# Kernel optimization log

Measured on AMD Instinct MI355X. Metric: run time of the kernel, lower is better.

Reference implementation:

```python
import jax, jax.numpy as jnp
import numpy as np

IDIM, HDIM, ODIM, G = 80, 512, 128, 5
B, T = 512, 512  # B = scan (time) axis of torch GRU (batch_first=False), T = GRU batch axis
P = G * 2 * ODIM + G  # 1285


def setup_inputs() -> dict:
    key = jax.random.key(0)
    ks = jax.random.split(key, 8)
    s = 0.05  # keep recurrent dynamics stable
    return {
        "ys": jax.random.normal(ks[0], (B, T, IDIM), jnp.float32),
        "W_ih": jax.random.normal(ks[1], (3 * HDIM, IDIM), jnp.float32) * s,
        "W_hh": jax.random.normal(ks[2], (3 * HDIM, HDIM), jnp.float32) * s,
        "b_ih": jax.random.normal(ks[3], (3 * HDIM,), jnp.float32) * s,
        "b_hh": jax.random.normal(ks[4], (3 * HDIM,), jnp.float32) * s,
        "W_proj": jax.random.normal(ks[5], (P, HDIM), jnp.float32) * s,
        "b_proj": jax.random.normal(ks[6], (P,), jnp.float32) * s,
        "eps": jax.random.normal(ks[7], (G, B, ODIM), jnp.float32),  # pre-drawn std-normal noise per component
    }


def _gru(ys, W_ih, W_hh, b_ih, b_hh):
    # torch GRU, batch_first=False: scan over axis 0 of ys, batch = axis 1.
    xp = jnp.einsum('btf,gf->btg', ys, W_ih) + b_ih  # (B, T, 3H), precomputed input projections
    h0 = jnp.zeros((ys.shape[1], HDIM), ys.dtype)

    def step(h, x):
        gh = h @ W_hh.T + b_hh
        xr, xz, xn = jnp.split(x, 3, axis=-1)
        hr, hz, hn = jnp.split(gh, 3, axis=-1)
        r = jax.nn.sigmoid(xr + hr)
        z = jax.nn.sigmoid(xz + hz)
        n = jnp.tanh(xn + r * hn)
        h_new = (1.0 - z) * n + z * h
        return h_new, h_new

    _, out = jax.lax.scan(step, h0, xp)  # (B, T, H)
    return out


def reference(ys, W_ih, W_hh, b_ih, b_hh, W_proj, b_proj, eps):
    out = _gru(ys, W_ih, W_hh, b_ih, b_hh)          # (B, T, H)
    last = out[:, -1, :]                             # (B, H), mirrors out[:, -1, :] in torch code
    params = last @ W_proj.T + b_proj                # (B, P)

    samples = jnp.zeros((ys.shape[0], ODIM), params.dtype)
    for i in range(G):  # tiny fixed component loop (G=5)
        mu = params[:, i * ODIM:(i + 1) * ODIM]                       # (B, odim)
        var = params[:, 2 * i * ODIM:(2 * i + 1) * ODIM] + 1e-6       # scale_tril diagonal == std
        s = jax.lax.stop_gradient(mu + var * eps[i])                  # MVN(mu, diag(var)^T diag(var)).sample()
        w = params[:, 2 * G * ODIM + i]                               # params[:, i - G]
        samples = samples + w[:, None] * s
    return samples[:, None, :]  # (B, 1, odim)
```

## Files before the change

### kernel.cpp

```cpp
#include <hip/hip_runtime.h>
#include <hip/hip_bf16.h>

#define IDIM 80
#define HDIM 512
#define ODIM 128
#define G5   5
#define BB   512
#define TT   512
#define PDIM 1285
#define GDIM 1536
#define NB   48
#define RPB  32

__device__ __forceinline__ void ag_store(float* p, float v) {
  __hip_atomic_store(p, v, __ATOMIC_RELAXED, __HIP_MEMORY_SCOPE_AGENT);
}
__device__ __forceinline__ float ag_load(const float* p) {
  return __hip_atomic_load(p, __ATOMIC_RELAXED, __HIP_MEMORY_SCOPE_AGENT);
}

__device__ __forceinline__ void grid_barrier(unsigned* bar, unsigned target) {
  __syncthreads();
  if (threadIdx.x == 0) {
    __hip_atomic_fetch_add(bar, 1u, __ATOMIC_ACQ_REL, __HIP_MEMORY_SCOPE_AGENT);
    while (__hip_atomic_load(bar, __ATOMIC_ACQUIRE, __HIP_MEMORY_SCOPE_AGENT) < target) {
      __builtin_amdgcn_s_sleep(1);
    }
  }
  __syncthreads();
}

__global__ void __launch_bounds__(512) gru_kernel(
    const float* __restrict__ ys, const float* __restrict__ W_ih,
    const float* __restrict__ W_hh, const float* __restrict__ b_ih,
    const float* __restrict__ b_hh,
    unsigned long long* ghT, float* xp, float* last, unsigned* bar)
{
  const int tid  = threadIdx.x;
  const int nb   = blockIdx.x;
  const int lane = tid & 63;
  const int wave = tid >> 6;
  const int r4   = lane >> 4;
  const int c    = lane & 15;
  const int row  = nb * RPB + wave * 4 + r4;

  __shared__ float hs[16 * 36];
  __shared__ float wih[32 * 82];
  __shared__ float bihs[32];

  float4 wreg[8];
  {
    const float4* wrow = (const float4*)(W_hh + (size_t)row * HDIM + c * 32);
    #pragma unroll
    for (int i = 0; i < 8; ++i) wreg[i] = wrow[i];
  }
  const float bhh_r = b_hh[row];

  for (int jj = tid; jj < 16 * 36; jj += 512) hs[jj] = 0.f;

  for (int idx = tid; idx < 32 * IDIM; idx += 512) {
    int g = idx / IDIM, f = idx % IDIM;
    wih[g * 82 + f] = W_ih[(size_t)(nb * RPB + g) * IDIM + f];
  }
  if (tid < 32) bihs[tid] = b_ih[nb * RPB + tid];
  __syncthreads();
  {
    const int g = tid & 31, b0 = tid >> 5;
    for (int pass = 0; pass < 32; ++pass) {
      int b = pass * 16 + b0;
      const float* yrow = ys + ((size_t)b * TT + (TT - 1)) * IDIM;
      float acc = bihs[g];
      #pragma unroll
      for (int f = 0; f < IDIM; f += 2) {
        float2 wv = *(const float2*)(&wih[g * 82 + f]);
        float2 yv = *(const float2*)(&yrow[f]);
        acc += wv.x * yv.x + wv.y * yv.y;
      }
      ag_store(&xp[(size_t)b * GDIM + nb * RPB + g], acc);
    }
  }
  grid_barrier(bar, NB * 1u);

  const int j = tid;
  const int jphys = (j >> 5) * 36 + (j & 31);

  for (int b = 0; b < BB; ++b) {
    const float* xpb = xp + (size_t)b * GDIM;
    float xr = ag_load(&xpb[j]);
    float xz = ag_load(&xpb[512 + j]);
    float xn = ag_load(&xpb[1024 + j]);

    const float4* hp = (const float4*)(hs + c * 36);
    float a0 = 0.f, a1 = 0.f, a2 = 0.f, a3 = 0.f;
    #pragma unroll
    for (int i = 0; i < 8; ++i) {
      float4 h4 = hp[i];
      a0 += wreg[i].x * h4.x; a1 += wreg[i].y * h4.y;
      a2 += wreg[i].z * h4.z; a3 += wreg[i].w * h4.w;
    }
    float acc = (a0 + a1) + (a2 + a3);
    acc += __shfl_xor(acc, 1);
    acc += __shfl_xor(acc, 2);
    acc += __shfl_xor(acc, 4);
    acc += __shfl_xor(acc, 8);
    unsigned long long* ghb = ghT + (size_t)(b & 1) * GDIM;
    if (c == 0) {
      union { float f; unsigned u; } cv; cv.f = acc + bhh_r;
      unsigned long long pv = ((unsigned long long)(unsigned)b << 32) | cv.u;
      __hip_atomic_store(&ghb[row], pv, __ATOMIC_RELAXED, __HIP_MEMORY_SCOPE_AGENT);
    }

    __syncthreads();

    float hr, hz, hn;
    {
      const unsigned long long* p0 = &ghb[j];
      const unsigned long long* p1 = &ghb[512 + j];
      const unsigned long long* p2 = &ghb[1024 + j];
      unsigned long long v0 = 0, v1 = 0, v2 = 0;
      bool d0 = false, d1 = false, d2 = false;
      int guard = 0;
      do {
        if (!d0) { v0 = __hip_atomic_load(p0, __ATOMIC_RELAXED, __HIP_MEMORY_SCOPE_AGENT);
                   d0 = ((unsigned)(v0 >> 32) == (unsigned)b); }
        if (!d1) { v1 = __hip_atomic_load(p1, __ATOMIC_RELAXED, __HIP_MEMORY_SCOPE_AGENT);
                   d1 = ((unsigned)(v1 >> 32) == (unsigned)b); }
        if (!d2) { v2 = __hip_atomic_load(p2, __ATOMIC_RELAXED, __HIP_MEMORY_SCOPE_AGENT);
                   d2 = ((unsigned)(v2 >> 32) == (unsigned)b); }
      } while ((!d0 || !d1 || !d2) && ++guard < (1 << 20));
      union { unsigned u; float f; } c0, c1, c2;
      c0.u = (unsigned)v0; c1.u = (unsigned)v1; c2.u = (unsigned)v2;
      hr = c0.f; hz = c1.f; hn = c2.f;
    }

    float h_old = hs[jphys];
    float r = 1.f / (1.f + __expf(-(xr + hr)));
    float z = 1.f / (1.f + __expf(-(xz + hz)));
    float e2 = __expf(2.f * (xn + r * hn));
    float n = 1.f - 2.f / (e2 + 1.f);
    float hnew = (1.f - z) * n + z * h_old;
    hs[jphys] = hnew;
    if (nb == 0) last[(size_t)b * HDIM + j] = hnew;
    __syncthreads();
  }
}

__global__ void __launch_bounds__(256) proj_kernel(
    const float* __restrict__ last, const float* __restrict__ W_proj,
    const float* __restrict__ b_proj, float* __restrict__ params)
{
  const int tid = threadIdx.x;
  const int pt = blockIdx.x * 64;
  const int bt = blockIdx.y * 64;
  __shared__ float As[16 * 65];
  __shared__ float Bs[16 * 65];
  const int tb = (tid >> 4) * 4;
  const int tp = (tid & 15) * 4;
  float acc[4][4] = {};
  for (int k0 = 0; k0 < HDIM; k0 += 16) {
    #pragma unroll
    for (int i = 0; i < 4; ++i) {
      int idx = tid + i * 256;
      int k = idx & 15, m = idx >> 4;
      As[k * 65 + m] = last[(size_t)(bt + m) * HDIM + k0 + k];
      int gp = pt + m;
      Bs[k * 65 + m] = (gp < PDIM) ? W_proj[(size_t)gp * HDIM + k0 + k] : 0.f;
    }
    __syncthreads();
    #pragma unroll
    for (int k = 0; k < 16; ++k) {
      float a[4], bv[4];
      #pragma unroll
      for (int i = 0; i < 4; ++i) a[i] = As[k * 65 + tb + i];
      #pragma unroll
      for (int i = 0; i < 4; ++i) bv[i] = Bs[k * 65 + tp + i];
      #pragma unroll
      for (int i = 0; i < 4; ++i)
        #pragma unroll
        for (int jj = 0; jj < 4; ++jj) acc[i][jj] += a[i] * bv[jj];
    }
    __syncthreads();
  }
  #pragma unroll
  for (int i = 0; i < 4; ++i) {
    int gb = bt + tb + i;
    #pragma unroll
    for (int jj = 0; jj < 4; ++jj) {
      int gp = pt + tp + jj;
      if (gp < PDIM) params[(size_t)gb * PDIM + gp] = acc[i][jj] + b_proj[gp];
    }
  }
}

__global__ void mix_kernel(const float* __restrict__ params,
                           const float* __restrict__ eps,
                           float* __restrict__ out)
{
  int b = blockIdx.x, o = threadIdx.x;
  const float* pr = params + (size_t)b * PDIM;
  float s = 0.f;
  #pragma unroll
  for (int i = 0; i < G5; ++i) {
    float mu  = pr[i * ODIM + o];
    float var = pr[2 * i * ODIM + o] + 1e-6f;
    float w   = pr[2 * G5 * ODIM + i];
    float e   = eps[((size_t)i * BB + b) * ODIM + o];
    s += w * (mu + var * e);
  }
  out[(size_t)b * ODIM + o] = s;
}

extern "C" void kernel_launch(void* const* d_in, const int* in_sizes, int n_in,
                              void* d_out, int out_size, void* d_ws, size_t ws_size,
                              hipStream_t stream) {
  const float* ys     = (const float*)d_in[0];
  const float* W_ih   = (const float*)d_in[1];
  const float* W_hh   = (const float*)d_in[2];
  const float* b_ih   = (const float*)d_in[3];
  const float* b_hh   = (const float*)d_in[4];
  const float* W_proj = (const float*)d_in[5];
  const float* b_proj = (const float*)d_in[6];
  const float* eps    = (const float*)d_in[7];
  float* out = (float*)d_out;

  char* ws = (char*)d_ws;
  unsigned* bar           = (unsigned*)ws;
  unsigned long long* ghT = (unsigned long long*)(ws + 256);
  float* xp     = (float*)(ws + 256 + 2 * GDIM * 8);
  float* last   = xp + (size_t)BB * GDIM;
  float* params = last + (size_t)BB * HDIM;

  hipMemsetAsync(bar, 0, 256, stream);
  hipMemsetAsync(ghT, 0xFF, 2 * GDIM * 8, stream);

  gru_kernel<<<NB, 512, 0, stream>>>(ys, W_ih, W_hh, b_ih, b_hh,
                                     ghT, xp, last, bar);

  dim3 gc((PDIM + 63) / 64, BB / 64);
  proj_kernel<<<gc, 256, 0, stream>>>(last, W_proj, b_proj, params);

  mix_kernel<<<BB, ODIM, 0, stream>>>(params, eps, out);
}
```

Before: 1.119 ms.

## Fuse output projection into GRU recurrence using double-buffered hidden state

Drops the separate projection GEMM kernel and the 'last' buffer. Each GRU block now holds a slice of W_proj rows in registers and computes params for the previous timestep from the shared hidden state while it waits for the cross-block gate exchange. The hidden state is double-buffered in shared memory, which lets one __syncthreads per step be removed. The cost is more registers and extra per-step work inside the latency-bound recurrence loop, which may lengthen the critical path.

```diff
diff --git a/kernel.cpp b/kernel.cpp
--- a/kernel.cpp
+++ b/kernel.cpp
@@ -11,11 +11,18 @@
 #define GDIM 1536
 #define NB   48
 #define RPB  32
-
-__device__ __forceinline__ void ag_store(float* p, float v) {
+#define PCPB 27
+
+__device__ __forceinline__ void ag_storef(float* p, float v) {
   __hip_atomic_store(p, v, __ATOMIC_RELAXED, __HIP_MEMORY_SCOPE_AGENT);
 }
-__device__ __forceinline__ float ag_load(const float* p) {
+__device__ __forceinline__ float ag_loadf(const float* p) {
+  return __hip_atomic_load(p, __ATOMIC_RELAXED, __HIP_MEMORY_SCOPE_AGENT);
+}
+__device__ __forceinline__ void ag_storeu(unsigned long long* p, unsigned long long v) {
+  __hip_atomic_store(p, v, __ATOMIC_RELAXED, __HIP_MEMORY_SCOPE_AGENT);
+}
+__device__ __forceinline__ unsigned long long ag_loadu(const unsigned long long* p) {
   return __hip_atomic_load(p, __ATOMIC_RELAXED, __HIP_MEMORY_SCOPE_AGENT);
 }
 
@@ -33,8 +40,10 @@
 __global__ void __launch_bounds__(512) gru_kernel(
     const float* __restrict__ ys, const float* __restrict__ W_ih,
     const float* __restrict__ W_hh, const float* __restrict__ b_ih,
-    const float* __restrict__ b_hh,
-    unsigned long long* ghT, float* xp, float* last, unsigned* bar)
+    const float* __restrict__ b_hh, const float* __restrict__ W_proj,
+    const float* __restrict__ b_proj,
+    float* __restrict__ xp, unsigned long long* __restrict__ ghT,
+    float* __restrict__ params, unsigned* __restrict__ bar)
 {
   const int tid  = threadIdx.x;
   const int nb   = blockIdx.x;
@@ -44,7 +53,7 @@
   const int c    = lane & 15;
   const int row  = nb * RPB + wave * 4 + r4;
 
-  __shared__ float hs[16 * 36];
+  __shared__ float hs[2][16 * 36];
   __shared__ float wih[32 * 82];
   __shared__ float bihs[32];
 
@@ -56,7 +65,19 @@
   }
   const float bhh_r = b_hh[row];
 
-  for (int jj = tid; jj < 16 * 36; jj += 512) hs[jj] = 0.f;
+  const int pcol = nb * PCPB + (tid >> 4);
+  const int pcl  = tid & 15;
+  const bool pact = (tid < 16 * PCPB) && (pcol < PDIM);
+  float4 wp[8] = {};
+  float bp = 0.f;
+  if (pact) {
+    const float4* wrow = (const float4*)(W_proj + (size_t)pcol * HDIM + pcl * 32);
+    #pragma unroll
+    for (int i = 0; i < 8; ++i) wp[i] = wrow[i];
+    bp = b_proj[pcol];
+  }
+
+  for (int w = tid; w < 16 * 36; w += 512) { hs[0][w] = 0.f; hs[1][w] = 0.f; }
 
   for (int idx = tid; idx < 32 * IDIM; idx += 512) {
     int g = idx / IDIM, f = idx % IDIM;
@@ -76,7 +97,7 @@
         float2 yv = *(const float2*)(&yrow[f]);
         acc += wv.x * yv.x + wv.y * yv.y;
       }
-      ag_store(&xp[(size_t)b * GDIM + nb * RPB + g], acc);
+      ag_storef(&xp[(size_t)b * GDIM + nb * RPB + g], acc);
     }
   }
   grid_barrier(bar, NB * 1u);
@@ -86,15 +107,15 @@
 
   for (int b = 0; b < BB; ++b) {
     const float* xpb = xp + (size_t)b * GDIM;
-    float xr = ag_load(&xpb[j]);
-    float xz = ag_load(&xpb[512 + j]);
-    float xn = ag_load(&xpb[1024 + j]);
-
-    const float4* hp = (const float4*)(hs + c * 36);
+    float xr = ag_loadf(&xpb[j]);
+    float xz = ag_loadf(&xpb[512 + j]);
+    float xn = ag_loadf(&xpb[1024 + j]);
+
+    const float* hbase = &hs[b & 1][c * 36];
     float a0 = 0.f, a1 = 0.f, a2 = 0.f, a3 = 0.f;
     #pragma unroll
     for (int i = 0; i < 8; ++i) {
-      float4 h4 = hp[i];
+      float4 h4 = ((const float4*)hbase)[i];
       a0 += wreg[i].x * h4.x; a1 += wreg[i].y * h4.y;
       a2 += wreg[i].z * h4.z; a3 += wreg[i].w * h4.w;
     }
@@ -107,10 +128,25 @@
     if (c == 0) {
       union { float f; unsigned u; } cv; cv.f = acc + bhh_r;
       unsigned long long pv = ((unsigned long long)(unsigned)b << 32) | cv.u;
-      __hip_atomic_store(&ghb[row], pv, __ATOMIC_RELAXED, __HIP_MEMORY_SCOPE_AGENT);
-    }
-
-    __syncthreads();
+      ag_storeu(&ghb[row], pv);
+    }
+
+    if (b >= 1 && pact) {
+      const float* pb = &hs[b & 1][pcl * 36];
+      float p0 = 0.f, p1 = 0.f, p2 = 0.f, p3 = 0.f;
+      #pragma unroll
+      for (int i = 0; i < 8; ++i) {
+        float4 h4 = ((const float4*)pb)[i];
+        p0 += wp[i].x * h4.x; p1 += wp[i].y * h4.y;
+        p2 += wp[i].z * h4.z; p3 += wp[i].w * h4.w;
+      }
+      float pr = (p0 + p1) + (p2 + p3);
+      pr += __shfl_xor(pr, 1);
+      pr += __shfl_xor(pr, 2);
+      pr += __shfl_xor(pr, 4);
+      pr += __shfl_xor(pr, 8);
+      if (pcl == 0) params[(size_t)(b - 1) * PDIM + pcol] = pr + bp;
+    }
 
     float hr, hz, hn;
     {
@@ -121,74 +157,40 @@
       bool d0 = false, d1 = false, d2 = false;
       int guard = 0;
       do {
-        if (!d0) { v0 = __hip_atomic_load(p0, __ATOMIC_RELAXED, __HIP_MEMORY_SCOPE_AGENT);
-                   d0 = ((unsigned)(v0 >> 32) == (unsigned)b); }
-        if (!d1) { v1 = __hip_atomic_load(p1, __ATOMIC_RELAXED, __HIP_MEMORY_SCOPE_AGENT);
-                   d1 = ((unsigned)(v1 >> 32) == (unsigned)b); }
-        if (!d2) { v2 = __hip_atomic_load(p2, __ATOMIC_RELAXED, __HIP_MEMORY_SCOPE_AGENT);
-                   d2 = ((unsigned)(v2 >> 32) == (unsigned)b); }
+        if (!d0) { v0 = ag_loadu(p0); d0 = ((unsigned)(v0 >> 32) == (unsigned)b); }
+        if (!d1) { v1 = ag_loadu(p1); d1 = ((unsigned)(v1 >> 32) == (unsigned)b); }
+        if (!d2) { v2 = ag_loadu(p2); d2 = ((unsigned)(v2 >> 32) == (unsigned)b); }
       } while ((!d0 || !d1 || !d2) && ++guard < (1 << 20));
       union { unsigned u; float f; } c0, c1, c2;
       c0.u = (unsigned)v0; c1.u = (unsigned)v1; c2.u = (unsigned)v2;
       hr = c0.f; hz = c1.f; hn = c2.f;
     }
 
-    float h_old = hs[jphys];
+    float h_old = hs[b & 1][jphys];
     float r = 1.f / (1.f + __expf(-(xr + hr)));
     float z = 1.f / (1.f + __expf(-(xz + hz)));
     float e2 = __expf(2.f * (xn + r * hn));
     float n = 1.f - 2.f / (e2 + 1.f);
     float hnew = (1.f - z) * n + z * h_old;
-    hs[jphys] = hnew;
-    if (nb == 0) last[(size_t)b * HDIM + j] = hnew;
+    hs[(b + 1) & 1][jphys] = hnew;
     __syncthreads();
   }
-}
-
-__global__ void __launch_bounds__(256) proj_kernel(
-    const float* __restrict__ last, const float* __restrict__ W_proj,
-    const float* __restrict__ b_proj, float* __restrict__ params)
-{
-  const int tid = threadIdx.x;
-  const int pt = blockIdx.x * 64;
-  const int bt = blockIdx.y * 64;
-  __shared__ float As[16 * 65];
-  __shared__ float Bs[16 * 65];
-  const int tb = (tid >> 4) * 4;
-  const int tp = (tid & 15) * 4;
-  float acc[4][4] = {};
-  for (int k0 = 0; k0 < HDIM; k0 += 16) {
-    #pragma unroll
-    for (int i = 0; i < 4; ++i) {
-      int idx = tid + i * 256;
-      int k = idx & 15, m = idx >> 4;
-      As[k * 65 + m] = last[(size_t)(bt + m) * HDIM + k0 + k];
-      int gp = pt + m;
-      Bs[k * 65 + m] = (gp < PDIM) ? W_proj[(size_t)gp * HDIM + k0 + k] : 0.f;
-    }
-    __syncthreads();
-    #pragma unroll
-    for (int k = 0; k < 16; ++k) {
-      float a[4], bv[4];
-      #pragma unroll
-      for (int i = 0; i < 4; ++i) a[i] = As[k * 65 + tb + i];
-      #pragma unroll
-      for (int i = 0; i < 4; ++i) bv[i] = Bs[k * 65 + tp + i];
-      #pragma unroll
-      for (int i = 0; i < 4; ++i)
-        #pragma unroll
-        for (int jj = 0; jj < 4; ++jj) acc[i][jj] += a[i] * bv[jj];
-    }
-    __syncthreads();
-  }
-  #pragma unroll
-  for (int i = 0; i < 4; ++i) {
-    int gb = bt + tb + i;
-    #pragma unroll
-    for (int jj = 0; jj < 4; ++jj) {
-      int gp = pt + tp + jj;
-      if (gp < PDIM) params[(size_t)gb * PDIM + gp] = acc[i][jj] + b_proj[gp];
-    }
+
+  if (pact) {
+    const float* pb = &hs[0][pcl * 36];
+    float p0 = 0.f, p1 = 0.f, p2 = 0.f, p3 = 0.f;
+    #pragma unroll
+    for (int i = 0; i < 8; ++i) {
+      float4 h4 = ((const float4*)pb)[i];
+      p0 += wp[i].x * h4.x; p1 += wp[i].y * h4.y;
+      p2 += wp[i].z * h4.z; p3 += wp[i].w * h4.w;
+    }
+    float pr = (p0 + p1) + (p2 + p3);
+    pr += __shfl_xor(pr, 1);
+    pr += __shfl_xor(pr, 2);
+    pr += __shfl_xor(pr, 4);
+    pr += __shfl_xor(pr, 8);
+    if (pcl == 0) params[(size_t)(BB - 1) * PDIM + pcol] = pr + bp;
   }
 }
 
@@ -227,17 +229,13 @@
   unsigned* bar           = (unsigned*)ws;
   unsigned long long* ghT = (unsigned long long*)(ws + 256);
   float* xp     = (float*)(ws + 256 + 2 * GDIM * 8);
-  float* last   = xp + (size_t)BB * GDIM;
-  float* params = last + (size_t)BB * HDIM;
+  float* params = xp + (size_t)BB * GDIM;
 
   hipMemsetAsync(bar, 0, 256, stream);
   hipMemsetAsync(ghT, 0xFF, 2 * GDIM * 8, stream);
 
   gru_kernel<<<NB, 512, 0, stream>>>(ys, W_ih, W_hh, b_ih, b_hh,
-                                     ghT, xp, last, bar);
-
-  dim3 gc((PDIM + 63) / 64, BB / 64);
-  proj_kernel<<<gc, 256, 0, stream>>>(last, W_proj, b_proj, params);
+                                     W_proj, b_proj, xp, ghT, params, bar);
 
   mix_kernel<<<BB, ODIM, 0, stream>>>(params, eps, out);
 }
```

Result: faster. 1.023 ms (-8.6%).
